# Kernel tuning notes

Measured on AMD Instinct MI355X. Metric: run time of the kernel, lower is better.

Reference implementation:

```python
import jax, jax.numpy as jnp
import numpy as np

B, T, S = 32, 64, 64
V, E, H, Hs = 32000, 512, 512, 512
D2 = 2 * Hs  # src feature dim


def setup_inputs() -> dict:
    key = jax.random.key(0)
    ks = jax.random.split(key, 26)
    n = lambda k, shape, s=0.05: (jax.random.normal(k, shape, jnp.float32) * s)
    inp = {
        'src': jax.random.normal(ks[0], (B, S, D2), jnp.float32),
        'trg': jax.random.randint(ks[1], (B, T), 0, V),
        'mask': jnp.ones((B, T), jnp.float32),
        'emb': n(ks[2], (V, E)),
        # PyTorch LSTMCell params: weight_ih [4H, E+H], weight_hh [4H, H]
        'f_Wih': n(ks[3], (4 * H, E + H)), 'f_Whh': n(ks[4], (4 * H, H)),
        'f_bih': n(ks[5], (4 * H,)), 'f_bhh': n(ks[6], (4 * H,)),
        'b_Wih': n(ks[7], (4 * H, E + H)), 'b_Whh': n(ks[8], (4 * H, H)),
        'b_bih': n(ks[9], (4 * H,)), 'b_bhh': n(ks[10], (4 * H,)),
        # attention projections: hidden -> 2*src_hidden
        'fatt_W': n(ks[11], (D2, H)), 'fatt_b': n(ks[12], (D2,)),
        'batt_W': n(ks[13], (D2, H)), 'batt_b': n(ks[14], (D2,)),
        # att_hidden linears: (H + 2*Hs) -> H
        'fah_W': n(ks[15], (H, H + D2)), 'fah_b': n(ks[16], (H,)),
        'bah_W': n(ks[17], (H, H + D2)), 'bah_b': n(ks[18], (H,)),
        # output projection 2H -> V
        'fc_W': n(ks[19], (V, 2 * H)), 'fc_b': n(ks[20], (V,)),
        'feed_init': n(ks[21], (2 * H,), 1.0),
        'hid_init': n(ks[22], (4 * H,), 1.0),
    }
    return inp


def reference(src, trg, mask, emb, f_Wih, f_Whh, f_bih, f_bhh,
              b_Wih, b_Whh, b_bih, b_bhh, fatt_W, fatt_b, batt_W, batt_b,
              fah_W, fah_b, bah_W, bah_b, fc_W, fc_b, feed_init, hid_init):
    Bn = src.shape[0]
    Hn = feed_init.shape[0] // 2
    scale = 1.0 / np.sqrt(Hn)  # key.size(-1) == trg hidden before projection

    x = emb[trg]  # [B, T, E]  (dropout p=0 -> identity)

    hhat0 = jnp.broadcast_to(feed_init, (Bn, 2 * Hn))
    f_hhat0, b_hhat0 = jnp.split(hhat0, 2, axis=1)
    hid0 = jnp.broadcast_to(hid_init, (Bn, 4 * Hn))
    f_hid, b_hid = jnp.split(hid0, 2, axis=-1)
    f_h0, f_c0 = jnp.split(f_hid, 2, axis=-1)
    b_h0, b_c0 = jnp.split(b_hid, 2, axis=-1)

    def lstm(xin, h, c, Wih, Whh, bih, bhh):
        g = xin @ Wih.T + bih + h @ Whh.T + bhh
        i, f, gg, o = jnp.split(g, 4, axis=-1)
        c = jax.nn.sigmoid(f) * c + jax.nn.sigmoid(i) * jnp.tanh(gg)
        h = jax.nn.sigmoid(o) * jnp.tanh(c)
        return h, c

    def att(h, W, b):
        k = h @ W.T + b                              # [B, 2Hs]
        w = jnp.einsum('bd,bsd->bs', k, src) * scale  # [B, S]
        p = jax.nn.softmax(w, axis=-1)
        return jnp.einsum('bs,bsd->bd', p, src)       # [B, 2Hs]

    xs = jnp.swapaxes(x, 0, 1)      # [T, B, E]
    ms = jnp.swapaxes(mask, 0, 1)   # [T, B]

    def f_step(carry, x_t):
        h, c, hhat = carry
        h, c = lstm(jnp.concatenate([x_t, hhat], -1), h, c, f_Wih, f_Whh, f_bih, f_bhh)
        ct = att(h, fatt_W, fatt_b)
        # NOTE: original uses b_att_hidden in the forward loop (faithful)
        hhat = jnp.tanh(jnp.concatenate([h, ct], -1) @ bah_W.T + bah_b)
        return (h, c, hhat), hhat

    _, f_out = jax.lax.scan(f_step, (f_h0, f_c0, f_hhat0), xs)  # [T, B, H]

    def b_step(carry, inp):
        x_t, m_t = inp
        h, c, hhat = carry
        hn, cn = lstm(jnp.concatenate([x_t, hhat], -1), h, c, b_Wih, b_Whh, b_bih, b_bhh)
        h = m_t[:, None] * hn
        c = m_t[:, None] * cn
        ct = att(h, batt_W, batt_b)
        # NOTE: original uses f_att_hidden in the backward loop (faithful)
        hhat = jnp.tanh(jnp.concatenate([h, ct], -1) @ fah_W.T + fah_b)
        return (h, c, hhat), hhat

    _, b_out = jax.lax.scan(b_step, (b_h0, b_c0, b_hhat0), (xs[::-1], ms[::-1]))

    f_out = jnp.swapaxes(f_out, 0, 1)        # [B, T, H]
    b_cheat = jnp.swapaxes(b_out, 0, 1)      # reversed-time order, as stacked in torch
    # b_outputs[:, :-2] = b_outputs_cheat[:, 2:]; last two steps zero (faithful)
    b_shift = jnp.concatenate([b_cheat[:, 2:], jnp.zeros_like(b_cheat[:, :2])], axis=1)

    logits = jnp.concatenate([f_out, b_shift], -1) @ fc_W.T + fc_b  # [B, T, V]
    return logits
```

## Files before the change

kernel.cpp:

```cpp
#include <hip/hip_runtime.h>
#include <hip/hip_bf16.h>
#include <math.h>

typedef __hip_bfloat16 bf16;
typedef __attribute__((ext_vector_type(8))) short short8b;
typedef __attribute__((ext_vector_type(8))) __bf16 bf16x8;
typedef __attribute__((ext_vector_type(4))) float f32x4;

#define SCALE_F 0.04419417382415922f

template <typename V>
static __device__ inline auto mfma_try(V a, V b, f32x4 c, int)
    -> decltype(__builtin_amdgcn_mfma_f32_16x16x32_bf16(a, b, c, 0, 0, 0)) {
  return __builtin_amdgcn_mfma_f32_16x16x32_bf16(a, b, c, 0, 0, 0);
}
template <typename V>
static __device__ inline auto mfma_try(V a, V b, f32x4 c, long)
    -> decltype(__builtin_amdgcn_mfma_f32_16x16x32_bf16(
        __builtin_bit_cast(bf16x8, a), __builtin_bit_cast(bf16x8, b), c, 0, 0, 0)) {
  return __builtin_amdgcn_mfma_f32_16x16x32_bf16(
      __builtin_bit_cast(bf16x8, a), __builtin_bit_cast(bf16x8, b), c, 0, 0, 0);
}
static __device__ inline f32x4 MFMA(short8b a, short8b b, f32x4 c) {
  return mfma_try(a, b, c, 0);
}

static __device__ inline short8b ldb8(const bf16* p) {
  return *reinterpret_cast<const short8b*>(p);
}
static __device__ inline float b2f(bf16 v) { return __bfloat162float(v); }
static __device__ inline bf16 f2b(float v) { return __float2bfloat16(v); }
static __device__ inline float s2f(short s) {
  unsigned u = ((unsigned)(unsigned short)s) << 16;
  return __builtin_bit_cast(float, u);
}
static __device__ inline unsigned pack2(float lo, float hi) {
  const unsigned a = (unsigned)__builtin_bit_cast(unsigned short, f2b(lo));
  const unsigned b = (unsigned)__builtin_bit_cast(unsigned short, f2b(hi));
  return a | (b << 16);
}
static __device__ inline float sigm(float x) { return 1.f / (1.f + expf(-x)); }

static __device__ inline void st2_wt(bf16* p, float v) {
  unsigned ud = (unsigned)__builtin_bit_cast(unsigned short, f2b(v));
  asm volatile("global_store_short %0, %1, off sc0 sc1" ::"v"(p), "v"(ud)
               : "memory");
}
static __device__ inline void st4_wt(bf16* p, float lo, float hi) {
  unsigned ud = pack2(lo, hi);
  asm volatile("global_store_dword %0, %1, off sc0 sc1" ::"v"(p), "v"(ud)
               : "memory");
}

static __device__ inline void st_flag(unsigned* p, unsigned v) {
  asm volatile("global_store_dword %0, %1, off sc0 sc1" ::"v"(p), "v"(v)
               : "memory");
}
static __device__ inline unsigned ld_flag(const unsigned* p) {
  unsigned v;
  asm volatile("global_load_dword %0, %1, off sc0 sc1\n\ts_waitcnt vmcnt(0)"
               : "=v"(v)
               : "v"(p)
               : "memory");
  return v;
}

static __device__ inline void gbar(unsigned* flags, unsigned ep, int blk, int tid) {
  asm volatile("s_waitcnt vmcnt(0)" ::: "memory");
  __syncthreads();
  if (tid < 64) {
    unsigned* row = flags + (size_t)ep * 64;
    if (tid == 0) st_flag(row + blk, 1u);
    while (true) {
      const unsigned v = ld_flag(row + tid);
      if (__ballot(v != 0) == ~0ull) break;
      __builtin_amdgcn_s_sleep(1);
    }
  }
  __syncthreads();
}

template <typename OutT, bool HAS_BIAS>
__global__ __launch_bounds__(256) void gemm_k(
    const bf16* __restrict__ A, const bf16* __restrict__ Bw,
    OutT* __restrict__ C, const float* __restrict__ bias,
    int M, int N, int K) {
  const int lane = threadIdx.x & 63;
  const int wid = threadIdx.x >> 6;
  const int m0 = blockIdx.y * 128 + (wid >> 1) * 64;
  const int n0 = blockIdx.x * 128 + (wid & 1) * 64;
  const int lr = lane & 15;
  const int lk = (lane >> 4) * 8;
  f32x4 acc[4][4];
#pragma unroll
  for (int i = 0; i < 4; ++i)
#pragma unroll
    for (int j = 0; j < 4; ++j) acc[i][j] = (f32x4){0.f, 0.f, 0.f, 0.f};
  const bf16* Ap = A + (size_t)(m0 + lr) * K + lk;
  const bf16* Bp = Bw + (size_t)(n0 + lr) * K + lk;
  for (int k0 = 0; k0 < K; k0 += 32) {
    short8b av[4], bv[4];
#pragma unroll
    for (int i = 0; i < 4; ++i) av[i] = ldb8(Ap + (size_t)i * 16 * K + k0);
#pragma unroll
    for (int i = 0; i < 4; ++i) bv[i] = ldb8(Bp + (size_t)i * 16 * K + k0);
#pragma unroll
    for (int mi = 0; mi < 4; ++mi)
#pragma unroll
      for (int ni = 0; ni < 4; ++ni)
        acc[mi][ni] = MFMA(av[mi], bv[ni], acc[mi][ni]);
  }
  const int rb = (lane >> 4) * 4;
#pragma unroll
  for (int mi = 0; mi < 4; ++mi) {
#pragma unroll
    for (int r = 0; r < 4; ++r) {
      const int row = m0 + mi * 16 + rb + r;
#pragma unroll
      for (int ni = 0; ni < 4; ++ni) {
        const int col = n0 + ni * 16 + lr;
        float v = acc[mi][ni][r];
        if (HAS_BIAS) v += bias[col];
        if constexpr (sizeof(OutT) == 2) {
          C[(size_t)row * N + col] = f2b(v);
        } else {
          C[(size_t)row * N + col] = v;
        }
      }
    }
  }
}

__global__ __launch_bounds__(256) void gemm_out(
    const bf16* __restrict__ A, const bf16* __restrict__ Bw,
    float* __restrict__ C, const float* __restrict__ bias) {
  constexpr int K = 1024, N = 32000;
  __shared__ bf16 As[128 * 32];
  __shared__ bf16 Bs[128 * 32];
  const int wgid = blockIdx.x;
  const int mt = wgid & 15, nt = wgid >> 4;
  const int tid = threadIdx.x, lane = tid & 63, wv = tid >> 6;
  const int m0 = mt * 128, n0 = nt * 128;
  const int lr16 = lane & 15, kb = lane >> 4, koff = kb * 8;
  const int r0 = tid >> 2, q0 = tid & 3;
  const int r1 = (tid + 256) >> 2;
  const bf16* Ap0 = A + (size_t)(m0 + r0) * K + q0 * 8;
  const bf16* Ap1 = A + (size_t)(m0 + r1) * K + q0 * 8;
  const bf16* Bp0 = Bw + (size_t)(n0 + r0) * K + q0 * 8;
  const bf16* Bp1 = Bw + (size_t)(n0 + r1) * K + q0 * 8;
  const int wm = (wv >> 1) * 64, wn = (wv & 1) * 64;
  f32x4 acc[4][4];
#pragma unroll
  for (int i = 0; i < 4; ++i)
#pragma unroll
    for (int j = 0; j < 4; ++j) acc[i][j] = (f32x4){0.f, 0.f, 0.f, 0.f};
  short8b a0 = ldb8(Ap0), a1 = ldb8(Ap1), b0 = ldb8(Bp0), b1 = ldb8(Bp1);
  for (int k0 = 0; k0 < K; k0 += 32) {
    __syncthreads();
    *reinterpret_cast<short8b*>(&As[tid * 8]) = a0;
    *reinterpret_cast<short8b*>(&As[(tid + 256) * 8]) = a1;
    *reinterpret_cast<short8b*>(&Bs[tid * 8]) = b0;
    *reinterpret_cast<short8b*>(&Bs[(tid + 256) * 8]) = b1;
    __syncthreads();
    if (k0 + 32 < K) {
      a0 = ldb8(Ap0 + k0 + 32);
      a1 = ldb8(Ap1 + k0 + 32);
      b0 = ldb8(Bp0 + k0 + 32);
      b1 = ldb8(Bp1 + k0 + 32);
    }
    short8b af[4], bfr[4];
#pragma unroll
    for (int i = 0; i < 4; ++i) {
      af[i] = *reinterpret_cast<const short8b*>(&As[(wm + i * 16 + lr16) * 32 + koff]);
      bfr[i] = *reinterpret_cast<const short8b*>(&Bs[(wn + i * 16 + lr16) * 32 + koff]);
    }
#pragma unroll
    for (int mi = 0; mi < 4; ++mi)
#pragma unroll
      for (int ni = 0; ni < 4; ++ni)
        acc[mi][ni] = MFMA(af[mi], bfr[ni], acc[mi][ni]);
  }
#pragma unroll
  for (int mi = 0; mi < 4; ++mi) {
#pragma unroll
    for (int r = 0; r < 4; ++r) {
      const int row = m0 + wm + mi * 16 + kb * 4 + r;
#pragma unroll
      for (int ni = 0; ni < 4; ++ni) {
        const int col = n0 + wn + ni * 16 + lr16;
        C[(size_t)row * N + col] = acc[mi][ni][r] + bias[col];
      }
    }
  }
}

__global__ void k_xg(const float* __restrict__ emb, const int* __restrict__ trg,
                     bf16* __restrict__ xg) {
  const int i = blockIdx.x * 256 + threadIdx.x;
  const int r = i >> 9, e = i & 511;
  const int t = r >> 5, b = r & 31;
  const int tok = trg[b * 64 + t];
  xg[i] = f2b(emb[(size_t)tok * 512 + e]);
}

__global__ void k_srcb(const float* __restrict__ s, bf16* __restrict__ d) {
  const int i = blockIdx.x * 256 + threadIdx.x;
  d[i] = f2b(s[i]);
}

__global__ void k_fcw(const float* __restrict__ s, bf16* __restrict__ d) {
  const size_t stride = (size_t)gridDim.x * blockDim.x;
  for (size_t i = blockIdx.x * (size_t)blockDim.x + threadIdx.x;
       i < (size_t)32000 * 1024; i += stride)
    d[i] = f2b(s[i]);
}

__global__ void k_bmt(const bf16* __restrict__ in, bf16* __restrict__ out) {
  const int i = blockIdx.x * 256 + threadIdx.x;
  const int b = i >> 15, rem = i & 32767, o = rem >> 6, s = rem & 63;
  out[i] = in[(size_t)(b * 64 + s) * 512 + o];
}

__global__ void k_wpack(const float* __restrict__ fWih, const float* __restrict__ fWhh,
                        const float* __restrict__ bWih, const float* __restrict__ bWhh,
                        const float* __restrict__ fattW, const float* __restrict__ battW,
                        const float* __restrict__ bahW, const float* __restrict__ fahW,
                        bf16* Wxf, bf16* Wxb, bf16* Wrecf, bf16* Wrecb,
                        bf16* attWtf, bf16* attWtb, bf16* ahW2f, bf16* ahW2b,
                        bf16* Wh1f, bf16* Wh1b) {
  const int stride = gridDim.x * blockDim.x;
  const int i0 = blockIdx.x * blockDim.x + threadIdx.x;
  for (int i = i0; i < 2048 * 512; i += stride) {
    const int gc = i >> 9, k = i & 511;
    Wxf[i] = f2b(fWih[(size_t)gc * 1024 + k]);
    Wxb[i] = f2b(bWih[(size_t)gc * 1024 + k]);
  }
  for (int i = i0; i < 2048 * 1024; i += stride) {
    const int gc = i >> 10, k = i & 1023;
    float vf, vb;
    if (k < 512) { vf = fWih[(size_t)gc * 1024 + 512 + k]; vb = bWih[(size_t)gc * 1024 + 512 + k]; }
    else         { vf = fWhh[(size_t)gc * 512 + k - 512]; vb = bWhh[(size_t)gc * 512 + k - 512]; }
    Wrecf[i] = f2b(vf); Wrecb[i] = f2b(vb);
  }
  for (int i = i0; i < 512 * 1024; i += stride) {
    const int j = i >> 10, d = i & 1023;
    attWtf[i] = f2b(fattW[(size_t)d * 512 + j]);
    attWtb[i] = f2b(battW[(size_t)d * 512 + j]);
  }
  for (int i = i0; i < 512 * 1024; i += stride) {
    const int o = i >> 10, d = i & 1023;
    ahW2f[i] = f2b(bahW[(size_t)o * 1536 + 512 + d]);
    ahW2b[i] = f2b(fahW[(size_t)o * 1536 + 512 + d]);
  }
  for (int i = i0; i < 512 * 512; i += stride) {
    const int o = i >> 9, k = i & 511;
    Wh1f[i] = f2b(bahW[(size_t)o * 1536 + k]);
    Wh1b[i] = f2b(fahW[(size_t)o * 1536 + k]);
  }
}

__global__ void k_c0(const float* __restrict__ src, const float* __restrict__ fb,
                     const float* __restrict__ bb, float* __restrict__ c0f,
                     float* __restrict__ c0b) {
  const int r = blockIdx.x;
  const int tid = threadIdx.x;
  float pf = 0.f, pb = 0.f;
  for (int d = tid; d < 1024; d += 256) {
    const float s = src[(size_t)r * 1024 + d];
    pf += s * fb[d];
    pb += s * bb[d];
  }
#pragma unroll
  for (int d = 1; d < 64; d <<= 1) { pf += __shfl_xor(pf, d); pb += __shfl_xor(pb, d); }
  __shared__ float rf[4], rb2[4];
  if ((tid & 63) == 0) { rf[tid >> 6] = pf; rb2[tid >> 6] = pb; }
  __syncthreads();
  if (tid == 0) {
    c0f[r] = (rf[0] + rf[1] + rf[2] + rf[3]) * SCALE_F;
    c0b[r] = (rb2[0] + rb2[1] + rb2[2] + rb2[3]) * SCALE_F;
  }
}

__global__ void k_init(const float* __restrict__ feed, const float* __restrict__ hid,
                       bf16* hh0, bf16* hh1, bf16* hb0, bf16* hb1,
                       float* cst0, float* cst1) {
  const int i = blockIdx.x * 256 + threadIdx.x;
  const int b = i >> 9, k = i & 511;
  hh0[i] = f2b(feed[k]);
  hh1[i] = f2b(feed[512 + k]);
  hb0[i] = f2b(hid[k]);
  hb1[i] = f2b(hid[1024 + k]);
  cst0[k * 32 + b] = hid[512 + k];
  cst1[k * 32 + b] = hid[1536 + k];
}

struct ScanP {
  const bf16* Wrec[2]; const bf16* Wx[2]; const bf16* xg;
  const bf16* Af[2]; const bf16* Bmt[2]; const bf16* Wh1[2];
  const float* bih[2]; const float* bhh[2];
  const float* c0[2]; const float* ahb[2]; const float* mask;
  bf16* hh[2]; bf16* hb[2]; bf16* U[2]; float* cst[2]; bf16* hcat; unsigned* flags;
};

__global__ __launch_bounds__(256) void scan_k(ScanP P) {
  const int blk = blockIdx.x;
  const int dir = blk >> 5;
  const int g = blk & 31;
  const int tid = threadIdx.x;
  const int lane = tid & 63;
  const int wv = tid >> 6;

  const bf16* __restrict__ Wrec = P.Wrec[dir];
  const bf16* __restrict__ Wx = P.Wx[dir];
  const bf16* __restrict__ xg = P.xg;
  const bf16* __restrict__ Af = P.Af[dir];
  const bf16* __restrict__ Bmt = P.Bmt[dir];
  const bf16* __restrict__ Wh1 = P.Wh1[dir];
  const float* __restrict__ bihp = P.bih[dir];
  const float* __restrict__ bhhp = P.bhh[dir];
  const float* __restrict__ c0v = P.c0[dir];
  const float* __restrict__ ahbp = P.ahb[dir];
  bf16* __restrict__ hhB = P.hh[dir];
  bf16* __restrict__ hbB = P.hb[dir];
  bf16* __restrict__ Ubuf = P.U[dir];
  float* __restrict__ cst = P.cst[dir];

  __shared__ float gl[4][16][33];
  __shared__ float h_lds[512];
  __shared__ float w_part[2][64];
  __shared__ float p_lds[64];

  unsigned ep = 0;
  const int lr16 = lane & 15;
  const int kb = lane >> 4;
  const int koff = kb * 8;

  short8b pA0[16], pA1[16];
  {
    const bf16* A0 = hbB + (size_t)lr16 * 512;
    const bf16* A1 = hbB + (size_t)(lr16 + 16) * 512;
#pragma unroll
    for (int ks = 0; ks < 16; ++ks) {
      pA0[ks] = ldb8(A0 + ks * 32 + koff);
      pA1[ks] = ldb8(A1 + ks * 32 + koff);
    }
  }

  for (int t = 0; t < 64; ++t) {
    const bf16* hhR = hhB + (size_t)t * 32 * 512;
    bf16* hhW = hhB + (size_t)(t + 1) * 32 * 512;
    bf16* hbW = hbB + (size_t)(t + 1) * 32 * 512;

    {
      const int gate = wv;
      const int gc = gate * 512 + g * 16 + lr16;
      const int tcol = dir ? (63 - t) : t;
      const bf16* Brow = Wrec + (size_t)gc * 1024;
      const bf16* Bxrow = Wx + (size_t)gc * 512;
      const bf16* A0h = hhR + (size_t)lr16 * 512;
      const bf16* A1h = hhR + (size_t)(lr16 + 16) * 512;
      const bf16* A0x = xg + ((size_t)tcol * 32 + lr16) * 512;
      const bf16* A1x = A0x + (size_t)16 * 512;
      f32x4 ac0 = (f32x4){0.f, 0.f, 0.f, 0.f};
      f32x4 ac1 = (f32x4){0.f, 0.f, 0.f, 0.f};
#pragma unroll
      for (int ks = 0; ks < 16; ++ks) {
        const int k = ks * 32 + koff;
        const short8b bv = ldb8(Brow + 512 + k);
        ac0 = MFMA(pA0[ks], bv, ac0);
        ac1 = MFMA(pA1[ks], bv, ac1);
      }
#pragma unroll
      for (int c = 0; c < 2; ++c) {
        short8b sa[8], sb[8];
#pragma unroll
        for (int i = 0; i < 8; ++i) {
          const int k = (c * 8 + i) * 32 + koff;
          sa[i] = ldb8(A0h + k);
          sb[i] = ldb8(A1h + k);
        }
#pragma unroll
        for (int i = 0; i < 8; ++i) {
          const int k = (c * 8 + i) * 32 + koff;
          const short8b bv = ldb8(Brow + k);
          ac0 = MFMA(sa[i], bv, ac0);
          ac1 = MFMA(sb[i], bv, ac1);
        }
      }
#pragma unroll
      for (int c = 0; c < 2; ++c) {
        short8b sa[8], sb[8];
#pragma unroll
        for (int i = 0; i < 8; ++i) {
          const int k = (c * 8 + i) * 32 + koff;
          sa[i] = ldb8(A0x + k);
          sb[i] = ldb8(A1x + k);
        }
#pragma unroll
        for (int i = 0; i < 8; ++i) {
          const int k = (c * 8 + i) * 32 + koff;
          const short8b bv = ldb8(Bxrow + k);
          ac0 = MFMA(sa[i], bv, ac0);
          ac1 = MFMA(sb[i], bv, ac1);
        }
      }
      const float bsum = bihp[gc] + bhhp[gc];
#pragma unroll
      for (int r = 0; r < 4; ++r) {
        const int brow = kb * 4 + r;
        gl[gate][lr16][brow] = ac0[r] + bsum;
        gl[gate][lr16][brow + 16] = ac1[r] + bsum;
      }
    }
    __syncthreads();
    {
      const int b = tid & 31;
      const int jp = (tid >> 5) * 2;
      float hn2[2];
#pragma unroll
      for (int u = 0; u < 2; ++u) {
        const int jl = jp + u;
        const int j = g * 16 + jl;
        const float gi = gl[0][jl][b];
        const float gf = gl[1][jl][b];
        const float gg = gl[2][jl][b];
        const float go = gl[3][jl][b];
        float cn = sigm(gf) * cst[j * 32 + b] + sigm(gi) * tanhf(gg);
        float hn = sigm(go) * tanhf(cn);
        if (dir) {
          const float m = P.mask[b * 64 + (63 - t)];
          hn *= m; cn *= m;
        }
        cst[j * 32 + b] = cn;
        hn2[u] = hn;
      }
      st4_wt(hbW + (size_t)b * 512 + g * 16 + jp, hn2[0], hn2[1]);
    }
    gbar(P.flags, ep++, blk, tid);

    if (wv == 0) {
      const bf16* Brow = Wh1 + (size_t)(g * 16 + lr16) * 512;
      const bf16* A0 = hbW + (size_t)lr16 * 512;
      const bf16* A1 = hbW + (size_t)(lr16 + 16) * 512;
      f32x4 u0 = (f32x4){0.f, 0.f, 0.f, 0.f};
      f32x4 u1 = (f32x4){0.f, 0.f, 0.f, 0.f};
#pragma unroll
      for (int ks = 0; ks < 16; ++ks) {
        const int k = ks * 32 + koff;
        const short8b bv = ldb8(Brow + k);
        u0 = MFMA(ldb8(A0 + k), bv, u0);
        u1 = MFMA(ldb8(A1 + k), bv, u1);
      }
      bf16* Uw = Ubuf + (size_t)t * 32 * 512;
      const int o = g * 16 + lr16;
#pragma unroll
      for (int r = 0; r < 4; ++r) {
        const int b0 = kb * 4 + r;
        st2_wt(Uw + (size_t)b0 * 512 + o, u0[r]);
        st2_wt(Uw + (size_t)(b0 + 16) * 512 + o, u1[r]);
      }
    } else if (wv == 1) {
      const short8b v = ldb8(hbW + (size_t)g * 512 + lane * 8);
#pragma unroll
      for (int e = 0; e < 8; ++e) h_lds[lane * 8 + e] = s2f(v[e]);
    }
    __syncthreads();
    if (wv == 1 || wv == 2) {
      const int q = wv - 1;
      const bf16* arow = Af + (size_t)(g * 64 + lane) * 512 + q * 256;
      float part = 0.f;
#pragma unroll 8
      for (int k8 = 0; k8 < 256; k8 += 8) {
        const short8b v = ldb8(arow + k8);
#pragma unroll
        for (int e = 0; e < 8; ++e) part += h_lds[q * 256 + k8 + e] * s2f(v[e]);
      }
      w_part[q][lane] = part;
    }
    __syncthreads();
    if (wv == 3) {
      const float v = (w_part[0][lane] + w_part[1][lane]) * SCALE_F + c0v[g * 64 + lane];
      float mx = v;
#pragma unroll
      for (int d = 1; d < 64; d <<= 1) mx = fmaxf(mx, __shfl_xor(mx, d));
      const float e = expf(v - mx);
      float sm = e;
#pragma unroll
      for (int d = 1; d < 64; d <<= 1) sm += __shfl_xor(sm, d);
      p_lds[lane] = e / sm;
    }
    __syncthreads();
    float a2[2];
    {
      const int o2 = tid * 2;
      const bf16* bm0 = Bmt + ((size_t)g * 512 + o2) * 64;
      short8b v0[8], v1[8];
#pragma unroll
      for (int i = 0; i < 8; ++i) {
        v0[i] = ldb8(bm0 + i * 8);
        v1[i] = ldb8(bm0 + 64 + i * 8);
      }
      float s0 = ahbp[o2], s1 = ahbp[o2 + 1];
#pragma unroll
      for (int i = 0; i < 8; ++i)
#pragma unroll
        for (int e = 0; e < 8; ++e) {
          const float p = p_lds[i * 8 + e];
          s0 += p * s2f(v0[i][e]);
          s1 += p * s2f(v1[i][e]);
        }
      a2[0] = s0; a2[1] = s1;
    }
    gbar(P.flags, ep++, blk, tid);

    {
      const int o2 = tid * 2;
      const unsigned uu =
          *reinterpret_cast<const unsigned*>(Ubuf + ((size_t)t * 32 + g) * 512 + o2);
      const float h0 = tanhf(a2[0] + s2f((short)(uu & 0xffffu)));
      const float h1 = tanhf(a2[1] + s2f((short)(uu >> 16)));
      st4_wt(hhW + (size_t)g * 512 + o2, h0, h1);
      const unsigned hp = pack2(h0, h1);
      if (dir == 0) {
        *reinterpret_cast<unsigned*>(P.hcat + (size_t)(g * 64 + t) * 1024 + o2) = hp;
      } else if (t >= 2) {
        *reinterpret_cast<unsigned*>(P.hcat + (size_t)(g * 64 + t - 2) * 1024 + 512 + o2) = hp;
      }
      if (t < 63) {
        const bf16* A0 = hbW + (size_t)lr16 * 512;
        const bf16* A1 = hbW + (size_t)(lr16 + 16) * 512;
#pragma unroll
        for (int ks = 0; ks < 16; ++ks) {
          pA0[ks] = ldb8(A0 + ks * 32 + koff);
          pA1[ks] = ldb8(A1 + ks * 32 + koff);
        }
      }
    }
    gbar(P.flags, ep++, blk, tid);
  }
}

extern "C" void kernel_launch(void* const* d_in, const int* in_sizes, int n_in,
                              void* d_out, int out_size, void* d_ws, size_t ws_size,
                              hipStream_t stream) {
  (void)in_sizes; (void)n_in; (void)out_size; (void)ws_size;
  const float* src  = (const float*)d_in[0];
  const int*   trg  = (const int*)d_in[1];
  const float* mask = (const float*)d_in[2];
  const float* emb  = (const float*)d_in[3];
  const float* fWih = (const float*)d_in[4];
  const float* fWhh = (const float*)d_in[5];
  const float* fbih = (const float*)d_in[6];
  const float* fbhh = (const float*)d_in[7];
  const float* bWih = (const float*)d_in[8];
  const float* bWhh = (const float*)d_in[9];
  const float* bbih = (const float*)d_in[10];
  const float* bbhh = (const float*)d_in[11];
  const float* fattW = (const float*)d_in[12];
  const float* fattb = (const float*)d_in[13];
  const float* battW = (const float*)d_in[14];
  const float* battb = (const float*)d_in[15];
  const float* fahW = (const float*)d_in[16];
  const float* fahb = (const float*)d_in[17];
  const float* bahW = (const float*)d_in[18];
  const float* bahb = (const float*)d_in[19];
  const float* fcW  = (const float*)d_in[20];
  const float* fcb  = (const float*)d_in[21];
  const float* feed = (const float*)d_in[22];
  const float* hid  = (const float*)d_in[23];

  char* wsp = (char*)d_ws;
  size_t off = 0;
  auto alloc = [&](size_t bytes) -> void* {
    void* p = wsp + off;
    off += (bytes + 255) & ~(size_t)255;
    return p;
  };
  unsigned* flags = (unsigned*)alloc((size_t)192 * 64 * 4);
  bf16* hcat = (bf16*)alloc((size_t)2048 * 1024 * 2);
  const size_t zero_bytes = off;
  bf16* xg    = (bf16*)alloc((size_t)2048 * 512 * 2);
  bf16* srcb  = (bf16*)alloc((size_t)2048 * 1024 * 2);
  bf16* fcWb  = (bf16*)alloc((size_t)32000 * 1024 * 2);
  bf16* Wxf   = (bf16*)alloc((size_t)2048 * 512 * 2);
  bf16* Wxb   = (bf16*)alloc((size_t)2048 * 512 * 2);
  bf16* Wrecf = (bf16*)alloc((size_t)2048 * 1024 * 2);
  bf16* Wrecb = (bf16*)alloc((size_t)2048 * 1024 * 2);
  bf16* attWtf = (bf16*)alloc((size_t)512 * 1024 * 2);
  bf16* attWtb = (bf16*)alloc((size_t)512 * 1024 * 2);
  bf16* ahW2f = (bf16*)alloc((size_t)512 * 1024 * 2);
  bf16* ahW2b = (bf16*)alloc((size_t)512 * 1024 * 2);
  bf16* Wh1f  = (bf16*)alloc((size_t)512 * 512 * 2);
  bf16* Wh1b  = (bf16*)alloc((size_t)512 * 512 * 2);
  bf16* Aff   = (bf16*)alloc((size_t)2048 * 512 * 2);
  bf16* Afb   = (bf16*)alloc((size_t)2048 * 512 * 2);
  bf16* Bmf   = (bf16*)alloc((size_t)2048 * 512 * 2);
  bf16* Bmb   = (bf16*)alloc((size_t)2048 * 512 * 2);
  bf16* Bmtf  = (bf16*)alloc((size_t)2048 * 512 * 2);
  bf16* Bmtb  = (bf16*)alloc((size_t)2048 * 512 * 2);
  float* c0f  = (float*)alloc(2048 * 4);
  float* c0b  = (float*)alloc(2048 * 4);
  bf16* hh0   = (bf16*)alloc((size_t)65 * 32 * 512 * 2);
  bf16* hh1   = (bf16*)alloc((size_t)65 * 32 * 512 * 2);
  bf16* hb0   = (bf16*)alloc((size_t)65 * 32 * 512 * 2);
  bf16* hb1   = (bf16*)alloc((size_t)65 * 32 * 512 * 2);
  bf16* Uf    = (bf16*)alloc((size_t)64 * 32 * 512 * 2);
  bf16* Ub    = (bf16*)alloc((size_t)64 * 32 * 512 * 2);
  float* cst0 = (float*)alloc((size_t)512 * 32 * 4);
  float* cst1 = (float*)alloc((size_t)512 * 32 * 4);

  hipMemsetAsync(d_ws, 0, zero_bytes, stream);

  k_xg<<<4096, 256, 0, stream>>>(emb, trg, xg);
  k_srcb<<<8192, 256, 0, stream>>>(src, srcb);
  k_fcw<<<8192, 256, 0, stream>>>(fcW, fcWb);
  k_wpack<<<2048, 256, 0, stream>>>(fWih, fWhh, bWih, bWhh, fattW, battW, bahW, fahW,
                                    Wxf, Wxb, Wrecf, Wrecb, attWtf, attWtb, ahW2f, ahW2b,
                                    Wh1f, Wh1b);
  k_c0<<<2048, 256, 0, stream>>>(src, fattb, battb, c0f, c0b);
  k_init<<<64, 256, 0, stream>>>(feed, hid, hh0, hh1, hb0, hb1, cst0, cst1);

  gemm_k<bf16, false><<<dim3(4, 16), 256, 0, stream>>>(srcb, attWtf, Aff, nullptr, 2048, 512, 1024);
  gemm_k<bf16, false><<<dim3(4, 16), 256, 0, stream>>>(srcb, attWtb, Afb, nullptr, 2048, 512, 1024);
  gemm_k<bf16, false><<<dim3(4, 16), 256, 0, stream>>>(srcb, ahW2f, Bmf, nullptr, 2048, 512, 1024);
  gemm_k<bf16, false><<<dim3(4, 16), 256, 0, stream>>>(srcb, ahW2b, Bmb, nullptr, 2048, 512, 1024);
  k_bmt<<<4096, 256, 0, stream>>>(Bmf, Bmtf);
  k_bmt<<<4096, 256, 0, stream>>>(Bmb, Bmtb);

  ScanP sp;
  sp.Wrec[0] = Wrecf; sp.Wrec[1] = Wrecb;
  sp.Wx[0] = Wxf;     sp.Wx[1] = Wxb;
  sp.xg = xg;
  sp.Af[0] = Aff;     sp.Af[1] = Afb;
  sp.Bmt[0] = Bmtf;   sp.Bmt[1] = Bmtb;
  sp.Wh1[0] = Wh1f;   sp.Wh1[1] = Wh1b;
  sp.bih[0] = fbih;   sp.bih[1] = bbih;
  sp.bhh[0] = fbhh;   sp.bhh[1] = bbhh;
  sp.c0[0] = c0f;     sp.c0[1] = c0b;
  sp.ahb[0] = bahb;   sp.ahb[1] = fahb;
  sp.mask = mask;
  sp.hh[0] = hh0;     sp.hh[1] = hh1;
  sp.hb[0] = hb0;     sp.hb[1] = hb1;
  sp.U[0] = Uf;       sp.U[1] = Ub;
  sp.cst[0] = cst0;   sp.cst[1] = cst1;
  sp.hcat = hcat;     sp.flags = flags;
  scan_k<<<64, 256, 0, stream>>>(sp);

  gemm_out<<<4000, 256, 0, stream>>>(hcat, fcWb, (float*)d_out, fcb);
}
```

Baseline: 2.941 ms.

## Precompute input-to-gate projections for all timesteps before the recurrent scan

Moves the embedding-input part of the LSTM gate matmul (x_t @ Wx^T) out of the sequential scan into two large batched GEMMs run beforehand, one per direction. Inside the scan each step now reads one precomputed bf16 value per gate element instead of doing 16 extra MFMA k-steps. This shortens the serial critical path of the latency-bound scan. In exchange it adds up-front GEMM work, 16 MB of workspace, and an extra bf16 rounding of the input projection.

```diff
diff --git a/kernel.cpp b/kernel.cpp
--- a/kernel.cpp
+++ b/kernel.cpp
@@ -295,9 +295,8 @@
 }
 
 struct ScanP {
-  const bf16* Wrec[2]; const bf16* Wx[2]; const bf16* xg;
-  const bf16* Af[2]; const bf16* Bmt[2]; const bf16* Wh1[2];
-  const float* bih[2]; const float* bhh[2];
+  const bf16* Wrec[2]; const bf16* Xp[2]; const bf16* Af[2]; const bf16* Bmt[2];
+  const bf16* Wh1[2]; const float* bih[2]; const float* bhh[2];
   const float* c0[2]; const float* ahb[2]; const float* mask;
   bf16* hh[2]; bf16* hb[2]; bf16* U[2]; float* cst[2]; bf16* hcat; unsigned* flags;
 };
@@ -311,8 +310,7 @@
   const int wv = tid >> 6;
 
   const bf16* __restrict__ Wrec = P.Wrec[dir];
-  const bf16* __restrict__ Wx = P.Wx[dir];
-  const bf16* __restrict__ xg = P.xg;
+  const bf16* __restrict__ Xp = P.Xp[dir];
   const bf16* __restrict__ Af = P.Af[dir];
   const bf16* __restrict__ Bmt = P.Bmt[dir];
   const bf16* __restrict__ Wh1 = P.Wh1[dir];
@@ -354,13 +352,9 @@
     {
       const int gate = wv;
       const int gc = gate * 512 + g * 16 + lr16;
-      const int tcol = dir ? (63 - t) : t;
       const bf16* Brow = Wrec + (size_t)gc * 1024;
-      const bf16* Bxrow = Wx + (size_t)gc * 512;
       const bf16* A0h = hhR + (size_t)lr16 * 512;
       const bf16* A1h = hhR + (size_t)(lr16 + 16) * 512;
-      const bf16* A0x = xg + ((size_t)tcol * 32 + lr16) * 512;
-      const bf16* A1x = A0x + (size_t)16 * 512;
       f32x4 ac0 = (f32x4){0.f, 0.f, 0.f, 0.f};
       f32x4 ac1 = (f32x4){0.f, 0.f, 0.f, 0.f};
 #pragma unroll
@@ -387,29 +381,14 @@
           ac1 = MFMA(sb[i], bv, ac1);
         }
       }
-#pragma unroll
-      for (int c = 0; c < 2; ++c) {
-        short8b sa[8], sb[8];
-#pragma unroll
-        for (int i = 0; i < 8; ++i) {
-          const int k = (c * 8 + i) * 32 + koff;
-          sa[i] = ldb8(A0x + k);
-          sb[i] = ldb8(A1x + k);
-        }
-#pragma unroll
-        for (int i = 0; i < 8; ++i) {
-          const int k = (c * 8 + i) * 32 + koff;
-          const short8b bv = ldb8(Bxrow + k);
-          ac0 = MFMA(sa[i], bv, ac0);
-          ac1 = MFMA(sb[i], bv, ac1);
-        }
-      }
+      const int tcol = dir ? (63 - t) : t;
       const float bsum = bihp[gc] + bhhp[gc];
+      const bf16* xpc = Xp + (size_t)gc * 2048 + tcol * 32;
 #pragma unroll
       for (int r = 0; r < 4; ++r) {
         const int brow = kb * 4 + r;
-        gl[gate][lr16][brow] = ac0[r] + bsum;
-        gl[gate][lr16][brow + 16] = ac1[r] + bsum;
+        gl[gate][lr16][brow] = ac0[r] + b2f(xpc[brow]) + bsum;
+        gl[gate][lr16][brow + 16] = ac1[r] + b2f(xpc[brow + 16]) + bsum;
       }
     }
     __syncthreads();
@@ -592,6 +571,8 @@
   bf16* ahW2b = (bf16*)alloc((size_t)512 * 1024 * 2);
   bf16* Wh1f  = (bf16*)alloc((size_t)512 * 512 * 2);
   bf16* Wh1b  = (bf16*)alloc((size_t)512 * 512 * 2);
+  bf16* Xpf   = (bf16*)alloc((size_t)2048 * 2048 * 2);
+  bf16* Xpb   = (bf16*)alloc((size_t)2048 * 2048 * 2);
   bf16* Aff   = (bf16*)alloc((size_t)2048 * 512 * 2);
   bf16* Afb   = (bf16*)alloc((size_t)2048 * 512 * 2);
   bf16* Bmf   = (bf16*)alloc((size_t)2048 * 512 * 2);
@@ -620,6 +601,8 @@
   k_c0<<<2048, 256, 0, stream>>>(src, fattb, battb, c0f, c0b);
   k_init<<<64, 256, 0, stream>>>(feed, hid, hh0, hh1, hb0, hb1, cst0, cst1);
 
+  gemm_k<bf16, false><<<dim3(16, 16), 256, 0, stream>>>(Wxf, xg, Xpf, nullptr, 2048, 2048, 512);
+  gemm_k<bf16, false><<<dim3(16, 16), 256, 0, stream>>>(Wxb, xg, Xpb, nullptr, 2048, 2048, 512);
   gemm_k<bf16, false><<<dim3(4, 16), 256, 0, stream>>>(srcb, attWtf, Aff, nullptr, 2048, 512, 1024);
   gemm_k<bf16, false><<<dim3(4, 16), 256, 0, stream>>>(srcb, attWtb, Afb, nullptr, 2048, 512, 1024);
   gemm_k<bf16, false><<<dim3(4, 16), 256, 0, stream>>>(srcb, ahW2f, Bmf, nullptr, 2048, 512, 1024);
@@ -629,8 +612,7 @@
 
   ScanP sp;
   sp.Wrec[0] = Wrecf; sp.Wrec[1] = Wrecb;
-  sp.Wx[0] = Wxf;     sp.Wx[1] = Wxb;
-  sp.xg = xg;
+  sp.Xp[0] = Xpf;     sp.Xp[1] = Xpb;
   sp.Af[0] = Aff;     sp.Af[1] = Afb;
   sp.Bmt[0] = Bmtf;   sp.Bmt[1] = Bmtb;
   sp.Wh1[0] = Wh1f;   sp.Wh1[1] = Wh1b;
```

Result: faster. 2.612 ms (-11.2%).
